# Performance work log

Hardware: AMD Instinct MI355X
Metric: run time of the kernel (lower is better)

## Reference

```python
import jax, jax.numpy as jnp
import numpy as np

B, T, V, H, E, MAX_OOV = 128, 200, 50257, 256, 128, 50


def setup_inputs() -> dict:
    key = jax.random.key(0)
    ks = jax.random.split(key, 17)
    s = 0.05  # param scale
    return {
        "decoder_input": jax.random.randint(ks[0], (B, 1), 0, V),
        "encoder_outputs": jax.random.normal(ks[1], (B, T, 2 * H), jnp.float32),
        "encoder_idxs": jax.random.randint(ks[2], (B, T), 0, V),
        "prev_state": jax.random.normal(ks[3], (1, B, H), jnp.float32),
        "selective_read": jax.random.normal(ks[4], (B, 1, 2 * H), jnp.float32) * s,
        "step": 1,
        "emb": jax.random.normal(ks[5], (V, E), jnp.float32) * s,
        "W_ih": jax.random.normal(ks[6], (3 * H, E + 2 * H), jnp.float32) * s,
        "W_hh": jax.random.normal(ks[7], (3 * H, H), jnp.float32) * s,
        "b_ih": jax.random.normal(ks[8], (3 * H,), jnp.float32) * s,
        "b_hh": jax.random.normal(ks[9], (3 * H,), jnp.float32) * s,
        "Wi_w": jax.random.normal(ks[10], (H, 2 * H), jnp.float32) * s,
        "Wi_b": jax.random.normal(ks[11], (H,), jnp.float32) * s,
        "Wg_w": jax.random.normal(ks[12], (V, H), jnp.float32) * s,
        "Wg_b": jax.random.normal(ks[13], (V,), jnp.float32) * s,
        "Wc_w": jax.random.normal(ks[14], (H, 2 * H), jnp.float32) * s,
        "Wc_b": jax.random.normal(ks[15], (H,), jnp.float32) * s,
    }


def _gru_cell(x, h, W_ih, W_hh, b_ih, b_hh):
    # torch GRUCell math, gate order r,z,n
    gi = x @ W_ih.T + b_ih
    gh = h @ W_hh.T + b_hh
    i_r, i_z, i_n = jnp.split(gi, 3, axis=-1)
    h_r, h_z, h_n = jnp.split(gh, 3, axis=-1)
    r = jax.nn.sigmoid(i_r + h_r)
    z = jax.nn.sigmoid(i_z + h_z)
    n = jnp.tanh(i_n + r * h_n)
    return (1.0 - z) * n + z * h


def reference(decoder_input, encoder_outputs, encoder_idxs, prev_state, selective_read,
              step, emb, W_ih, W_hh, b_ih, b_hh, Wi_w, Wi_b, Wg_w, Wg_b, Wc_w, Wc_b):
    dtype = encoder_outputs.dtype
    if step == 0:
        prev_state = (encoder_outputs[:, -1] @ Wi_w.T + Wi_b)[None]      # 1,B,H
        selective_read = jnp.zeros((B, 1, 2 * H), dtype)
    embedded = emb[decoder_input[:, 0]]                                   # B,E
    gru_in = jnp.concatenate([selective_read[:, 0], embedded], axis=-1)   # B,2H+E
    decode_hidden = _gru_cell(gru_in, prev_state[0], W_ih, W_hh, b_ih, b_hh)  # B,H

    score_g = decode_hidden @ Wg_w.T + Wg_b                               # B,V
    enc_proj = jnp.tanh(jnp.einsum('bte,he->bth', encoder_outputs, Wc_w) + Wc_b)  # B,T,H
    score_c = jnp.tanh(jnp.einsum('bth,bh->bt', enc_proj, decode_hidden))         # B,T
    score_c = score_c + jnp.where(encoder_idxs == 0, -10000.0, 0.0).astype(dtype)

    probs = jax.nn.softmax(jnp.concatenate([score_g, score_c], axis=1), axis=1)   # B,V+T
    prob_g, prob_c = probs[:, :V], probs[:, V:]
    prob_g = jnp.concatenate([prob_g, jnp.full((B, MAX_OOV), 1e-4, dtype)], axis=1)  # B,V+oov

    # copy-distribution aggregation: scatter-add prob_c by vocab id (replaces one-hot bmm)
    prob_c_to_g = jnp.zeros((B, V + MAX_OOV), dtype).at[
        jnp.arange(B)[:, None], encoder_idxs].add(prob_c)
    prob_out = (prob_c_to_g + prob_g)[:, None, :]                          # B,1,V+oov

    # selective read for next step
    match = (encoder_idxs == decoder_input).astype(dtype)                  # B,T
    tot = match.sum(axis=1, keepdims=True)
    match = jnp.where(tot > 1, match / tot, match)
    prob_appeared = prob_c * match
    selective_read_new = jnp.einsum('bt,bte->be', prob_appeared, encoder_outputs)[:, None, :]  # B,1,2H
    return prob_out, decode_hidden, selective_read_new
```

## Files before the change

### kernel.cpp

```cpp
#include <hip/hip_runtime.h>

typedef __bf16 bf16;
typedef __bf16 bf16x4 __attribute__((ext_vector_type(4)));
typedef __bf16 bf16x8 __attribute__((ext_vector_type(8)));
typedef float f32x4 __attribute__((ext_vector_type(4)));

#define B_ 128
#define T_ 200
#define V_ 50257
#define H_ 256
#define E_ 128
#define OOV_ 50
#define VO_ 50307
#define NRG 64
#define NTS 4
#define GSC 786
#define NROWP 50304
#define PSTR 800
#define PBSTR 50368
#define GPJ 800

__device__ __forceinline__ float sigmoid_(float x) { return 1.0f / (1.0f + __expf(-x)); }
__device__ __forceinline__ float tanh_(float x) { return 1.0f - 2.0f / (__expf(2.0f * x) + 1.0f); }

__global__ void k_front(const float* Wc_w, bf16* WcPack,
                        const int* step_p, const float* enc, const float* prev,
                        const float* selread, const int* dec, const float* emb,
                        const float* Wi_w, const float* Wi_b,
                        float* hT, float* ginT,
                        const float* Wg_w, bf16* WgPack) {
    if (blockIdx.x < 128) {
        int gid = blockIdx.x * 256 + threadIdx.x;
        int n = gid >> 7;
        int k = (gid & 127) * 4;
        float4 v = *(const float4*)(Wc_w + n * 512 + k);
        int kstep = k >> 5, kin = k & 31;
        int q = kin >> 3, j0 = kin & 7;
        int r = n & 15, nt = n >> 4;
        int lane = q * 16 + r;
        bf16* d = WcPack + (((nt * 16 + kstep) * 64) + lane) * 8 + j0;
        d[0] = (bf16)v.x; d[1] = (bf16)v.y; d[2] = (bf16)v.z; d[3] = (bf16)v.w;
    } else if (blockIdx.x < 256) {
        int b = blockIdx.x - 128, t = threadIdx.x;
        int step = step_p[0];
        float h;
        if (step == 0) {
            float acc = Wi_b[t];
            const float* er = enc + (b * T_ + (T_ - 1)) * 512;
            const float* wr = Wi_w + t * 512;
            for (int k = 0; k < 512; ++k) acc += er[k] * wr[k];
            h = acc;
        } else {
            h = prev[b * H_ + t];
        }
        hT[t * B_ + b] = h;
        for (int k = t; k < 512; k += 256)
            ginT[k * B_ + b] = (step == 0) ? 0.0f : selread[b * 512 + k];
        if (t < E_)
            ginT[(512 + t) * B_ + b] = emb[dec[b] * E_ + t];
    } else {
        int pb = blockIdx.x - 256;
        int t = threadIdx.x;
        int w = t >> 6, lane = t & 63;
        int r = lane & 15, q = lane >> 4;
        int nt = pb * 4 + w;
        int row = nt * 16 + r;
        bool valid = (row < V_);
        const float* src = Wg_w + (size_t)(valid ? row : (V_ - 1)) * 256 + q * 8;
        bf16* dst = WgPack + ((size_t)(nt * 8) * 64 + lane) * 8;
#pragma unroll
        for (int ks = 0; ks < 8; ++ks) {
            float4 va = *(const float4*)(src + ks * 32);
            float4 vb = *(const float4*)(src + ks * 32 + 4);
            bf16x8 o;
            if (valid) {
                o[0] = (bf16)va.x; o[1] = (bf16)va.y; o[2] = (bf16)va.z; o[3] = (bf16)va.w;
                o[4] = (bf16)vb.x; o[5] = (bf16)vb.y; o[6] = (bf16)vb.z; o[7] = (bf16)vb.w;
            } else {
                o[0] = o[1] = o[2] = o[3] = o[4] = o[5] = o[6] = o[7] = (bf16)0.0f;
            }
            *(bf16x8*)(dst + (size_t)ks * 512) = o;
        }
    }
}

__global__ void k_gemm_gru(const float* W_ih, const float* b_ih,
                           const float* W_hh, const float* b_hh,
                           const float* ginT, const float* hT,
                           float* giT, float* ghT) {
    __shared__ float red[256];
    int rrow = blockIdx.x;
    int t = threadIdx.x;
    int b = t & 127, kh = t >> 7;
    const float* w = W_ih + rrow * 640 + kh * 320;
    const float* g = ginT + (kh * 320) * B_ + b;
    float a0 = 0.f, a1 = 0.f, a2 = 0.f, a3 = 0.f;
#pragma unroll 4
    for (int k = 0; k < 320; k += 4) {
        a0 += w[k]     * g[k * B_];
        a1 += w[k + 1] * g[(k + 1) * B_];
        a2 += w[k + 2] * g[(k + 2) * B_];
        a3 += w[k + 3] * g[(k + 3) * B_];
    }
    const float* w2 = W_hh + rrow * 256 + kh * 128;
    const float* hh = hT + (kh * 128) * B_ + b;
    float c0 = 0.f, c1 = 0.f, c2 = 0.f, c3 = 0.f;
#pragma unroll 4
    for (int k = 0; k < 128; k += 4) {
        c0 += w2[k]     * hh[k * B_];
        c1 += w2[k + 1] * hh[(k + 1) * B_];
        c2 += w2[k + 2] * hh[(k + 2) * B_];
        c3 += w2[k + 3] * hh[(k + 3) * B_];
    }
    red[t] = ((a0 + a1) + (a2 + a3));
    __syncthreads();
    if (kh == 0) giT[rrow * B_ + b] = b_ih[rrow] + red[b] + red[b + 128];
    __syncthreads();
    red[t] = ((c0 + c1) + (c2 + c3));
    __syncthreads();
    if (kh == 0) ghT[rrow * B_ + b] = b_hh[rrow] + red[b] + red[b + 128];
}

__global__ void k_gru_cell(const float* giT, const float* ghT, const float* hT,
                           float* out_dh, bf16* Apack) {
    int b = blockIdx.x, j = threadIdx.x;
    float ir = giT[j * B_ + b], iz = giT[(256 + j) * B_ + b], in_ = giT[(512 + j) * B_ + b];
    float hr = ghT[j * B_ + b], hz = ghT[(256 + j) * B_ + b], hn = ghT[(512 + j) * B_ + b];
    float hp = hT[j * B_ + b];
    float r = sigmoid_(ir + hr);
    float z = sigmoid_(iz + hz);
    float n = tanh_(in_ + r * hn);
    float h = (1.0f - z) * n + z * hp;
    out_dh[b * H_ + j] = h;
    int mt = b >> 4, rr = b & 15, ks = j >> 5, q = (j >> 3) & 3, jj = j & 7;
    Apack[(((mt * 8 + ks) * 64) + (q * 16 + rr)) * 8 + jj] = (bf16)h;
}

__global__ __launch_bounds__(512, 2) void k_score(const bf16* Apack, const bf16* WgPack,
                                                  const float* Wg_b,
                                                  bf16* expg, float* pg_part) {
    int tid = threadIdx.x;
    int w = tid >> 6, lane = tid & 63;
    int r = lane & 15, q = lane >> 4;
    int blk = blockIdx.x;
    int n0 = blk * NRG;
    const bf16* bbase = WgPack + (size_t)(blk * NTS * 8) * 512 + lane * 8;
    const bf16* abase = Apack + (w * 8) * 512 + lane * 8;
    f32x4 acc[NTS];
#pragma unroll
    for (int i = 0; i < NTS; ++i) acc[i] = (f32x4){0.f, 0.f, 0.f, 0.f};
#pragma unroll
    for (int ks = 0; ks < 8; ++ks) {
        bf16x8 a = *(const bf16x8*)(abase + ks * 512);
#pragma unroll
        for (int nt = 0; nt < NTS; ++nt) {
            bf16x8 bfr = *(const bf16x8*)(bbase + (nt * 8 + ks) * 512);
            acc[nt] = __builtin_amdgcn_mfma_f32_16x16x32_bf16(a, bfr, acc[nt], 0, 0, 0);
        }
    }
    float rsum[4] = {0.f, 0.f, 0.f, 0.f};
#pragma unroll
    for (int nt = 0; nt < NTS; ++nt) {
        int n = n0 + nt * 16 + r;
        bool valid = (n < V_);
        float wgb = Wg_b[valid ? n : (V_ - 1)];
#pragma unroll
        for (int rg = 0; rg < 4; ++rg) {
            int row = w * 16 + q * 4 + rg;
            float e = valid ? __expf(acc[nt][rg] + wgb) : 0.0f;
            rsum[rg] += e;
            expg[row * PBSTR + n] = (bf16)e;
        }
    }
#pragma unroll
    for (int rg = 0; rg < 4; ++rg) {
        float s = rsum[rg];
        s += __shfl_xor(s, 1);
        s += __shfl_xor(s, 2);
        s += __shfl_xor(s, 4);
        s += __shfl_xor(s, 8);
        if (r == 0) {
            int row = w * 16 + q * 4 + rg;
            pg_part[row * PSTR + blk] = s;
        }
    }
}

__global__ __launch_bounds__(256, 4) void k_proj(const float* enc, const bf16* WcPack,
                                                 const float* Wc_b, const float* dh,
                                                 const int* idxs, float* expc) {
    __shared__ unsigned char smem[17408];
    int tid = threadIdx.x;
    int w = tid >> 6, lane = tid & 63;
    int r = lane & 15, q = lane >> 4;
    int m0 = blockIdx.x * 32;
    bf16* As = (bf16*)smem;
    float* sred = (float*)(smem + 16896);
    f32x4 acc[8];
#pragma unroll
    for (int i = 0; i < 8; ++i) acc[i] = (f32x4){0.f, 0.f, 0.f, 0.f};
    for (int half = 0; half < 2; ++half) {
        __syncthreads();
#pragma unroll
        for (int ph = 0; ph < 2; ++ph) {
            float4 tmp[4];
#pragma unroll
            for (int j = 0; j < 4; ++j) {
                int f = (ph * 4 + j) * 256 + tid;
                int row = f >> 6, c4 = f & 63;
                tmp[j] = *(const float4*)(enc + (m0 + row) * 512 + half * 256 + c4 * 4);
            }
#pragma unroll
            for (int j = 0; j < 4; ++j) {
                int f = (ph * 4 + j) * 256 + tid;
                int row = f >> 6, c4 = f & 63;
                bf16x4 o;
                o[0] = (bf16)tmp[j].x; o[1] = (bf16)tmp[j].y;
                o[2] = (bf16)tmp[j].z; o[3] = (bf16)tmp[j].w;
                *(bf16x4*)(As + row * 264 + c4 * 4) = o;
            }
        }
        __syncthreads();
#pragma unroll
        for (int ks = 0; ks < 8; ++ks) {
            int kstep = half * 8 + ks;
            bf16x8 bfr[4];
#pragma unroll
            for (int ntl = 0; ntl < 4; ++ntl)
                bfr[ntl] = *(const bf16x8*)(WcPack + (((w * 4 + ntl) * 16 + kstep) * 64 + lane) * 8);
#pragma unroll
            for (int mt = 0; mt < 2; ++mt) {
                bf16x8 a = *(const bf16x8*)(As + (mt * 16 + r) * 264 + ks * 32 + q * 8);
#pragma unroll
                for (int ntl = 0; ntl < 4; ++ntl)
                    acc[mt * 4 + ntl] = __builtin_amdgcn_mfma_f32_16x16x32_bf16(a, bfr[ntl], acc[mt * 4 + ntl], 0, 0, 0);
            }
        }
    }
#pragma unroll
    for (int mt = 0; mt < 2; ++mt) {
#pragma unroll
        for (int rg = 0; rg < 4; ++rg) {
            int rowl = mt * 16 + q * 4 + rg;
            int row = m0 + rowl;
            int b = row / T_;
            float s = 0.0f;
#pragma unroll
            for (int ntl = 0; ntl < 4; ++ntl) {
                int n = (w * 4 + ntl) * 16 + r;
                float pv = tanh_(acc[mt * 4 + ntl][rg] + Wc_b[n]);
                s += pv * dh[b * H_ + n];
            }
            s += __shfl_xor(s, 1);
            s += __shfl_xor(s, 2);
            s += __shfl_xor(s, 4);
            s += __shfl_xor(s, 8);
            if (r == 0) sred[rowl * 4 + w] = s;
        }
    }
    __syncthreads();
    if (tid < 32) {
        float s = sred[tid * 4] + sred[tid * 4 + 1] + sred[tid * 4 + 2] + sred[tid * 4 + 3];
        int row = m0 + tid;
        int b = row / T_, t = row - b * T_;
        float sc = tanh_(s);
        if (idxs[b * T_ + t] == 0) sc -= 10000.0f;
        expc[row] = __expf(sc);
    }
}

__global__ void k_reduce(const float* pg_part, const float* expc_, const int* idxs,
                         const int* dec, const float* enc, float* inv_out,
                         float* out_sel) {
    __shared__ float red[256];
    __shared__ float cf[256];
    int b = blockIdx.x, t = threadIdx.x;
    float s = 0.0f;
    for (int i = t; i < GSC; i += 256) s += pg_part[b * PSTR + i];
    if (t < T_) s += expc_[b * T_ + t];
    red[t] = s;
    __syncthreads();
    for (int k = 128; k > 0; k >>= 1) {
        if (t < k) red[t] += red[t + k];
        __syncthreads();
    }
    float iv = 1.0f / red[0];
    if (t == 0) inv_out[b] = iv;
    __syncthreads();
    int d = dec[b];
    float ec = 0.0f;
    int m = 0;
    if (t < T_) {
        int ix = idxs[b * T_ + t];
        ec = expc_[b * T_ + t];
        m = (ix == d) ? 1 : 0;
    }
    cf[t] = m ? ec * iv : 0.0f;
    red[t] = m ? 1.0f : 0.0f;
    __syncthreads();
    for (int k = 128; k > 0; k >>= 1) {
        if (t < k) red[t] += red[t + k];
        __syncthreads();
    }
    float tot = red[0];
    float scale = (tot > 1.0f) ? 1.0f / tot : 1.0f;
    float a0 = 0.0f, a1 = 0.0f;
    for (int tt = 0; tt < T_; ++tt) {
        float c = cf[tt];
        if (c != 0.0f) {
            float wgt = c * scale;
            a0 += wgt * enc[(b * T_ + tt) * 512 + t];
            a1 += wgt * enc[(b * T_ + tt) * 512 + t + 256];
        }
    }
    out_sel[b * 512 + t] = a0;
    out_sel[b * 512 + t + 256] = a1;
}

__global__ __launch_bounds__(256) void k_normwrite(const bf16* expg, const float* inv,
                                                   float* out_prob) {
    int b = blockIdx.x >> 5, c = blockIdx.x & 31;
    int t = threadIdx.x;
    float iv = inv[b];
    int base = b * VO_;
    const bf16* eg = expg + b * PBSTR;
    int i4s = (base + 3) >> 2;
    int i4e = (base + VO_) >> 2;
    int head = (i4s << 2) - base;
    if (c == 0 && t < head) {
        int col = t;
        out_prob[base + col] = (float)eg[col] * iv;
    }
    int tail = (base + VO_) - (i4e << 2);
    if (c == 31 && t < tail) {
        int col = (i4e << 2) - base + t;
        out_prob[base + col] = (col < V_) ? (float)eg[col] * iv : 1e-4f;
    }
    int n4 = i4e - i4s;
    int per = (n4 + 31) >> 5;
    int s0 = i4s + c * per;
    int e0 = s0 + per; if (e0 > i4e) e0 = i4e;
    int sh = (4 - (base & 3)) & 3;
    for (int i4 = s0 + t; i4 < e0; i4 += 256) {
        int col = (i4 << 2) - base;
        int al = col & ~3;
        bf16x4 L0 = *(const bf16x4*)(eg + al);
        bf16x4 L1 = *(const bf16x4*)(eg + al + 4);
        float f0 = (float)L0[0], f1 = (float)L0[1], f2 = (float)L0[2], f3 = (float)L0[3];
        float f4 = (float)L1[0], f5 = (float)L1[1], f6 = (float)L1[2];
        float v0, v1, v2, v3;
        if (sh == 0)      { v0 = f0; v1 = f1; v2 = f2; v3 = f3; }
        else if (sh == 1) { v0 = f1; v1 = f2; v2 = f3; v3 = f4; }
        else if (sh == 2) { v0 = f2; v1 = f3; v2 = f4; v3 = f5; }
        else              { v0 = f3; v1 = f4; v2 = f5; v3 = f6; }
        float o0 = (col + 0 < V_) ? v0 * iv : 1e-4f;
        float o1 = (col + 1 < V_) ? v1 * iv : 1e-4f;
        float o2 = (col + 2 < V_) ? v2 * iv : 1e-4f;
        float o3 = (col + 3 < V_) ? v3 * iv : 1e-4f;
        *(float4*)(out_prob + (i4 << 2)) = make_float4(o0, o1, o2, o3);
    }
}

__global__ void k_scatter(const float* expc_, const int* idxs, const float* inv,
                          float* out_prob) {
    int b = blockIdx.x, t = threadIdx.x;
    if (t < T_) {
        int ix = idxs[b * T_ + t];
        atomicAdd(&out_prob[b * VO_ + ix], expc_[b * T_ + t] * inv[b]);
    }
}

extern "C" void kernel_launch(void* const* d_in, const int* in_sizes, int n_in,
                              void* d_out, int out_size, void* d_ws, size_t ws_size,
                              hipStream_t stream) {
    const int*   dec     = (const int*)d_in[0];
    const float* enc     = (const float*)d_in[1];
    const int*   idxs    = (const int*)d_in[2];
    const float* prev    = (const float*)d_in[3];
    const float* selread = (const float*)d_in[4];
    const int*   step_p  = (const int*)d_in[5];
    const float* emb     = (const float*)d_in[6];
    const float* W_ih    = (const float*)d_in[7];
    const float* W_hh    = (const float*)d_in[8];
    const float* b_ih    = (const float*)d_in[9];
    const float* b_hh    = (const float*)d_in[10];
    const float* Wi_w    = (const float*)d_in[11];
    const float* Wi_b    = (const float*)d_in[12];
    const float* Wg_w    = (const float*)d_in[13];
    const float* Wg_b    = (const float*)d_in[14];
    const float* Wc_w    = (const float*)d_in[15];
    const float* Wc_b    = (const float*)d_in[16];

    float* ws     = (float*)d_ws;
    float* hT     = ws;
    float* ginT   = ws + 32768;
    float* giT    = ws + 114688;
    float* ghT    = ws + 212992;
    float* inv    = ws + 311296;
    float* expc   = ws + 311552;
    float* pgp    = ws + 337152;
    bf16*  Apack  = (bf16*)(ws + 741376);
    bf16*  WcPack = (bf16*)(ws + 757760);
    bf16*  expg   = (bf16*)(ws + 823296);

    float* out      = (float*)d_out;
    float* out_prob = out;
    float* out_dh   = out + 6439296;
    float* out_sel  = out + 6439296 + 32768;
    bf16*  WgPack   = (bf16*)out;

    k_front<<<256 + GSC, 256, 0, stream>>>(Wc_w, WcPack, step_p, enc, prev, selread,
                                           dec, emb, Wi_w, Wi_b, hT, ginT,
                                           Wg_w, WgPack);
    k_gemm_gru<<<768, 256, 0, stream>>>(W_ih, b_ih, W_hh, b_hh, ginT, hT, giT, ghT);
    k_gru_cell<<<B_, 256, 0, stream>>>(giT, ghT, hT, out_dh, Apack);
    k_proj<<<GPJ, 256, 0, stream>>>(enc, WcPack, Wc_b, out_dh, idxs, expc);
    k_score<<<GSC, 512, 0, stream>>>(Apack, WgPack, Wg_b, expg, pgp);
    k_reduce<<<B_, 256, 0, stream>>>(pgp, expc, idxs, dec, enc, inv, out_sel);
    k_normwrite<<<B_ * 32, 256, 0, stream>>>(expg, inv, out_prob);
    k_scatter<<<B_, 256, 0, stream>>>(expc, idxs, inv, out_prob);
}
```

Baseline: 271.1 us.

## Distribute Wg bf16 packing blocks across gemm, gru cell and proj launches

Removes the Wg_w bf16 packing blocks from the front kernel and appends them as extra blocks to the GRU gemm, GRU cell and projection kernels, split 200/36/550. This fills the idle CUs in those small launches with the independent packing work instead of running it up front. The cost is extra memory bandwidth contention with the projection kernel, whose main work is also bandwidth-bound.

```diff
diff --git a/kernel.cpp b/kernel.cpp
--- a/kernel.cpp
+++ b/kernel.cpp
@@ -19,16 +19,41 @@
 #define PSTR 800
 #define PBSTR 50368
 #define GPJ 800
+#define PK_GEMM 200
+#define PK_CELL 36
+#define PK_PROJ 550
 
 __device__ __forceinline__ float sigmoid_(float x) { return 1.0f / (1.0f + __expf(-x)); }
 __device__ __forceinline__ float tanh_(float x) { return 1.0f - 2.0f / (__expf(2.0f * x) + 1.0f); }
+
+__device__ __forceinline__ void pack_wg(int pb, int t, const float* Wg_w, bf16* WgPack) {
+    int w = t >> 6, lane = t & 63;
+    int r = lane & 15, q = lane >> 4;
+    int nt = pb * 4 + w;
+    int row = nt * 16 + r;
+    bool valid = (row < V_);
+    const float* src = Wg_w + (size_t)(valid ? row : (V_ - 1)) * 256 + q * 8;
+    bf16* dst = WgPack + ((size_t)(nt * 8) * 64 + lane) * 8;
+#pragma unroll
+    for (int ks = 0; ks < 8; ++ks) {
+        float4 va = *(const float4*)(src + ks * 32);
+        float4 vb = *(const float4*)(src + ks * 32 + 4);
+        bf16x8 o;
+        if (valid) {
+            o[0] = (bf16)va.x; o[1] = (bf16)va.y; o[2] = (bf16)va.z; o[3] = (bf16)va.w;
+            o[4] = (bf16)vb.x; o[5] = (bf16)vb.y; o[6] = (bf16)vb.z; o[7] = (bf16)vb.w;
+        } else {
+            o[0] = o[1] = o[2] = o[3] = o[4] = o[5] = o[6] = o[7] = (bf16)0.0f;
+        }
+        *(bf16x8*)(dst + (size_t)ks * 512) = o;
+    }
+}
 
 __global__ void k_front(const float* Wc_w, bf16* WcPack,
                         const int* step_p, const float* enc, const float* prev,
                         const float* selread, const int* dec, const float* emb,
                         const float* Wi_w, const float* Wi_b,
-                        float* hT, float* ginT,
-                        const float* Wg_w, bf16* WgPack) {
+                        float* hT, float* ginT) {
     if (blockIdx.x < 128) {
         int gid = blockIdx.x * 256 + threadIdx.x;
         int n = gid >> 7;
@@ -40,7 +65,7 @@
         int lane = q * 16 + r;
         bf16* d = WcPack + (((nt * 16 + kstep) * 64) + lane) * 8 + j0;
         d[0] = (bf16)v.x; d[1] = (bf16)v.y; d[2] = (bf16)v.z; d[3] = (bf16)v.w;
-    } else if (blockIdx.x < 256) {
+    } else {
         int b = blockIdx.x - 128, t = threadIdx.x;
         int step = step_p[0];
         float h;
@@ -58,37 +83,19 @@
             ginT[k * B_ + b] = (step == 0) ? 0.0f : selread[b * 512 + k];
         if (t < E_)
             ginT[(512 + t) * B_ + b] = emb[dec[b] * E_ + t];
-    } else {
-        int pb = blockIdx.x - 256;
-        int t = threadIdx.x;
-        int w = t >> 6, lane = t & 63;
-        int r = lane & 15, q = lane >> 4;
-        int nt = pb * 4 + w;
-        int row = nt * 16 + r;
-        bool valid = (row < V_);
-        const float* src = Wg_w + (size_t)(valid ? row : (V_ - 1)) * 256 + q * 8;
-        bf16* dst = WgPack + ((size_t)(nt * 8) * 64 + lane) * 8;
-#pragma unroll
-        for (int ks = 0; ks < 8; ++ks) {
-            float4 va = *(const float4*)(src + ks * 32);
-            float4 vb = *(const float4*)(src + ks * 32 + 4);
-            bf16x8 o;
-            if (valid) {
-                o[0] = (bf16)va.x; o[1] = (bf16)va.y; o[2] = (bf16)va.z; o[3] = (bf16)va.w;
-                o[4] = (bf16)vb.x; o[5] = (bf16)vb.y; o[6] = (bf16)vb.z; o[7] = (bf16)vb.w;
-            } else {
-                o[0] = o[1] = o[2] = o[3] = o[4] = o[5] = o[6] = o[7] = (bf16)0.0f;
-            }
-            *(bf16x8*)(dst + (size_t)ks * 512) = o;
-        }
     }
 }
 
 __global__ void k_gemm_gru(const float* W_ih, const float* b_ih,
                            const float* W_hh, const float* b_hh,
                            const float* ginT, const float* hT,
-                           float* giT, float* ghT) {
+                           float* giT, float* ghT,
+                           const float* Wg_w, bf16* WgPack) {
     __shared__ float red[256];
+    if (blockIdx.x >= 768) {
+        pack_wg(blockIdx.x - 768, threadIdx.x, Wg_w, WgPack);
+        return;
+    }
     int rrow = blockIdx.x;
     int t = threadIdx.x;
     int b = t & 127, kh = t >> 7;
@@ -122,7 +129,12 @@
 }
 
 __global__ void k_gru_cell(const float* giT, const float* ghT, const float* hT,
-                           float* out_dh, bf16* Apack) {
+                           float* out_dh, bf16* Apack,
+                           const float* Wg_w, bf16* WgPack) {
+    if (blockIdx.x >= 128) {
+        pack_wg(PK_GEMM + (blockIdx.x - 128), threadIdx.x, Wg_w, WgPack);
+        return;
+    }
     int b = blockIdx.x, j = threadIdx.x;
     float ir = giT[j * B_ + b], iz = giT[(256 + j) * B_ + b], in_ = giT[(512 + j) * B_ + b];
     float hr = ghT[j * B_ + b], hz = ghT[(256 + j) * B_ + b], hn = ghT[(512 + j) * B_ + b];
@@ -136,6 +148,94 @@
     Apack[(((mt * 8 + ks) * 64) + (q * 16 + rr)) * 8 + jj] = (bf16)h;
 }
 
+__global__ __launch_bounds__(256, 4) void k_proj(const float* enc, const bf16* WcPack,
+                                                 const float* Wc_b, const float* dh,
+                                                 const int* idxs, float* expc,
+                                                 const float* Wg_w, bf16* WgPack) {
+    __shared__ unsigned char smem[17408];
+    if (blockIdx.x >= GPJ) {
+        pack_wg(PK_GEMM + PK_CELL + (blockIdx.x - GPJ), threadIdx.x, Wg_w, WgPack);
+        return;
+    }
+    int tid = threadIdx.x;
+    int w = tid >> 6, lane = tid & 63;
+    int r = lane & 15, q = lane >> 4;
+    int m0 = blockIdx.x * 32;
+    bf16* As = (bf16*)smem;
+    float* sred = (float*)(smem + 16896);
+    f32x4 acc[8];
+#pragma unroll
+    for (int i = 0; i < 8; ++i) acc[i] = (f32x4){0.f, 0.f, 0.f, 0.f};
+    for (int half = 0; half < 2; ++half) {
+        __syncthreads();
+#pragma unroll
+        for (int ph = 0; ph < 2; ++ph) {
+            float4 tmp[4];
+#pragma unroll
+            for (int j = 0; j < 4; ++j) {
+                int f = (ph * 4 + j) * 256 + tid;
+                int row = f >> 6, c4 = f & 63;
+                tmp[j] = *(const float4*)(enc + (m0 + row) * 512 + half * 256 + c4 * 4);
+            }
+#pragma unroll
+            for (int j = 0; j < 4; ++j) {
+                int f = (ph * 4 + j) * 256 + tid;
+                int row = f >> 6, c4 = f & 63;
+                bf16x4 o;
+                o[0] = (bf16)tmp[j].x; o[1] = (bf16)tmp[j].y;
+                o[2] = (bf16)tmp[j].z; o[3] = (bf16)tmp[j].w;
+                *(bf16x4*)(As + row * 264 + c4 * 4) = o;
+            }
+        }
+        __syncthreads();
+#pragma unroll
+        for (int ks = 0; ks < 8; ++ks) {
+            int kstep = half * 8 + ks;
+            bf16x8 bfr[4];
+#pragma unroll
+            for (int ntl = 0; ntl < 4; ++ntl)
+                bfr[ntl] = *(const bf16x8*)(WcPack + (((w * 4 + ntl) * 16 + kstep) * 64 + lane) * 8);
+#pragma unroll
+            for (int mt = 0; mt < 2; ++mt) {
+                bf16x8 a = *(const bf16x8*)(As + (mt * 16 + r) * 264 + ks * 32 + q * 8);
+#pragma unroll
+                for (int ntl = 0; ntl < 4; ++ntl)
+                    acc[mt * 4 + ntl] = __builtin_amdgcn_mfma_f32_16x16x32_bf16(a, bfr[ntl], acc[mt * 4 + ntl], 0, 0, 0);
+            }
+        }
+    }
+#pragma unroll
+    for (int mt = 0; mt < 2; ++mt) {
+#pragma unroll
+        for (int rg = 0; rg < 4; ++rg) {
+            int rowl = mt * 16 + q * 4 + rg;
+            int row = m0 + rowl;
+            int b = row / T_;
+            float s = 0.0f;
+#pragma unroll
+            for (int ntl = 0; ntl < 4; ++ntl) {
+                int n = (w * 4 + ntl) * 16 + r;
+                float pv = tanh_(acc[mt * 4 + ntl][rg] + Wc_b[n]);
+                s += pv * dh[b * H_ + n];
+            }
+            s += __shfl_xor(s, 1);
+            s += __shfl_xor(s, 2);
+            s += __shfl_xor(s, 4);
+            s += __shfl_xor(s, 8);
+            if (r == 0) sred[rowl * 4 + w] = s;
+        }
+    }
+    __syncthreads();
+    if (tid < 32) {
+        float s = sred[tid * 4] + sred[tid * 4 + 1] + sred[tid * 4 + 2] + sred[tid * 4 + 3];
+        int row = m0 + tid;
+        int b = row / T_, t = row - b * T_;
+        float sc = tanh_(s);
+        if (idxs[b * T_ + t] == 0) sc -= 10000.0f;
+        expc[row] = __expf(sc);
+    }
+}
+
 __global__ __launch_bounds__(512, 2) void k_score(const bf16* Apack, const bf16* WgPack,
                                                   const float* Wg_b,
                                                   bf16* expg, float* pg_part) {
@@ -183,89 +283,6 @@
             int row = w * 16 + q * 4 + rg;
             pg_part[row * PSTR + blk] = s;
         }
-    }
-}
-
-__global__ __launch_bounds__(256, 4) void k_proj(const float* enc, const bf16* WcPack,
-                                                 const float* Wc_b, const float* dh,
-                                                 const int* idxs, float* expc) {
-    __shared__ unsigned char smem[17408];
-    int tid = threadIdx.x;
-    int w = tid >> 6, lane = tid & 63;
-    int r = lane & 15, q = lane >> 4;
-    int m0 = blockIdx.x * 32;
-    bf16* As = (bf16*)smem;
-    float* sred = (float*)(smem + 16896);
-    f32x4 acc[8];
-#pragma unroll
-    for (int i = 0; i < 8; ++i) acc[i] = (f32x4){0.f, 0.f, 0.f, 0.f};
-    for (int half = 0; half < 2; ++half) {
-        __syncthreads();
-#pragma unroll
-        for (int ph = 0; ph < 2; ++ph) {
-            float4 tmp[4];
-#pragma unroll
-            for (int j = 0; j < 4; ++j) {
-                int f = (ph * 4 + j) * 256 + tid;
-                int row = f >> 6, c4 = f & 63;
-                tmp[j] = *(const float4*)(enc + (m0 + row) * 512 + half * 256 + c4 * 4);
-            }
-#pragma unroll
-            for (int j = 0; j < 4; ++j) {
-                int f = (ph * 4 + j) * 256 + tid;
-                int row = f >> 6, c4 = f & 63;
-                bf16x4 o;
-                o[0] = (bf16)tmp[j].x; o[1] = (bf16)tmp[j].y;
-                o[2] = (bf16)tmp[j].z; o[3] = (bf16)tmp[j].w;
-                *(bf16x4*)(As + row * 264 + c4 * 4) = o;
-            }
-        }
-        __syncthreads();
-#pragma unroll
-        for (int ks = 0; ks < 8; ++ks) {
-            int kstep = half * 8 + ks;
-            bf16x8 bfr[4];
-#pragma unroll
-            for (int ntl = 0; ntl < 4; ++ntl)
-                bfr[ntl] = *(const bf16x8*)(WcPack + (((w * 4 + ntl) * 16 + kstep) * 64 + lane) * 8);
-#pragma unroll
-            for (int mt = 0; mt < 2; ++mt) {
-                bf16x8 a = *(const bf16x8*)(As + (mt * 16 + r) * 264 + ks * 32 + q * 8);
-#pragma unroll
-                for (int ntl = 0; ntl < 4; ++ntl)
-                    acc[mt * 4 + ntl] = __builtin_amdgcn_mfma_f32_16x16x32_bf16(a, bfr[ntl], acc[mt * 4 + ntl], 0, 0, 0);
-            }
-        }
-    }
-#pragma unroll
-    for (int mt = 0; mt < 2; ++mt) {
-#pragma unroll
-        for (int rg = 0; rg < 4; ++rg) {
-            int rowl = mt * 16 + q * 4 + rg;
-            int row = m0 + rowl;
-            int b = row / T_;
-            float s = 0.0f;
-#pragma unroll
-            for (int ntl = 0; ntl < 4; ++ntl) {
-                int n = (w * 4 + ntl) * 16 + r;
-                float pv = tanh_(acc[mt * 4 + ntl][rg] + Wc_b[n]);
-                s += pv * dh[b * H_ + n];
-            }
-            s += __shfl_xor(s, 1);
-            s += __shfl_xor(s, 2);
-            s += __shfl_xor(s, 4);
-            s += __shfl_xor(s, 8);
-            if (r == 0) sred[rowl * 4 + w] = s;
-        }
-    }
-    __syncthreads();
-    if (tid < 32) {
-        float s = sred[tid * 4] + sred[tid * 4 + 1] + sred[tid * 4 + 2] + sred[tid * 4 + 3];
-        int row = m0 + tid;
-        int b = row / T_, t = row - b * T_;
-        float sc = tanh_(s);
-        if (idxs[b * T_ + t] == 0) sc -= 10000.0f;
-        expc[row] = __expf(sc);
     }
 }
 
@@ -409,12 +426,14 @@
     float* out_sel  = out + 6439296 + 32768;
     bf16*  WgPack   = (bf16*)out;
 
-    k_front<<<256 + GSC, 256, 0, stream>>>(Wc_w, WcPack, step_p, enc, prev, selread,
-                                           dec, emb, Wi_w, Wi_b, hT, ginT,
-                                           Wg_w, WgPack);
-    k_gemm_gru<<<768, 256, 0, stream>>>(W_ih, b_ih, W_hh, b_hh, ginT, hT, giT, ghT);
-    k_gru_cell<<<B_, 256, 0, stream>>>(giT, ghT, hT, out_dh, Apack);
-    k_proj<<<GPJ, 256, 0, stream>>>(enc, WcPack, Wc_b, out_dh, idxs, expc);
+    k_front<<<256, 256, 0, stream>>>(Wc_w, WcPack, step_p, enc, prev, selread,
+                                     dec, emb, Wi_w, Wi_b, hT, ginT);
+    k_gemm_gru<<<768 + PK_GEMM, 256, 0, stream>>>(W_ih, b_ih, W_hh, b_hh, ginT, hT,
+                                                  giT, ghT, Wg_w, WgPack);
+    k_gru_cell<<<128 + PK_CELL, 256, 0, stream>>>(giT, ghT, hT, out_dh, Apack,
+                                                  Wg_w, WgPack);
+    k_proj<<<GPJ + PK_PROJ, 256, 0, stream>>>(enc, WcPack, Wc_b, out_dh, idxs, expc,
+                                              Wg_w, WgPack);
     k_score<<<GSC, 512, 0, stream>>>(Apack, WgPack, Wg_b, expg, pgp);
     k_reduce<<<B_, 256, 0, stream>>>(pgp, expc, idxs, dec, enc, inv, out_sel);
     k_normwrite<<<B_ * 32, 256, 0, stream>>>(expg, inv, out_prob);
```

Result: no change. 272.1 us (+0.4%).
